# Kernel tuning notes

Hardware: AMD Instinct MI355X
Metric: run time of the kernel (lower is better)

The kernel has to match this reference:

```python
import jax, jax.numpy as jnp
import numpy as np

N_NODES = 50000
N_EDGES = 600000
IC, H, OC = 64, 128, 32
EPS = 1e-5


def setup_inputs() -> dict:
    key = jax.random.key(0)
    ks = jax.random.split(key, 8)
    x = jax.random.normal(ks[0], (N_NODES, IC), dtype=jnp.float32)
    ei = jax.random.randint(ks[1], (2, N_EDGES), 0, N_NODES, dtype=jnp.int64)
    proj_w = jax.random.normal(ks[2], (IC, H), dtype=jnp.float32) * 0.05
    proj_b = jnp.zeros((H,), dtype=jnp.float32)
    # conv_w[layer, lin, :, :] with lin order: key, query, value, skip
    conv_w = jax.random.normal(ks[3], (3, 4, H, H), dtype=jnp.float32) * 0.05
    conv_b = jnp.zeros((3, 4, H), dtype=jnp.float32)
    bn_gamma = jnp.ones((3, H), dtype=jnp.float32)
    bn_beta = jnp.zeros((3, H), dtype=jnp.float32)
    head_w = jax.random.normal(ks[4], (H, OC), dtype=jnp.float32) * 0.05
    head_b = jnp.zeros((OC,), dtype=jnp.float32)
    return {"x": x, "ei": ei, "proj_w": proj_w, "proj_b": proj_b,
            "conv_w": conv_w, "conv_b": conv_b, "bn_gamma": bn_gamma,
            "bn_beta": bn_beta, "head_w": head_w, "head_b": head_b}


def _res_gated_conv(x, src, dst, w, b):
    # PyG ResGatedGraphConv: out_i = skip(x_i) + sum_j sigmoid(key(x_i)+query(x_j)) * value(x_j)
    k = x @ w[0] + b[0]      # key   (applied to target/dst)
    q = x @ w[1] + b[1]      # query (applied to source/src)
    v = x @ w[2] + b[2]      # value (applied to source/src)
    msg = jax.nn.sigmoid(k[dst] + q[src]) * v[src]          # [E, H]
    agg = jax.ops.segment_sum(msg, dst, num_segments=x.shape[0])  # [N, H]
    return x @ w[3] + b[3] + agg


def _batchnorm(x, gamma, beta):
    # training-mode BatchNorm1d: batch statistics over the node dimension
    mean = jnp.mean(x, axis=0)
    var = jnp.var(x, axis=0)
    return gamma * (x - mean) * jax.lax.rsqrt(var + EPS) + beta


def reference(x, ei, proj_w, proj_b, conv_w, conv_b, bn_gamma, bn_beta, head_w, head_b):
    src, dst = ei[0], ei[1]
    h = jax.nn.relu(x @ proj_w + proj_b)
    for layer in range(3):
        h = _res_gated_conv(h, src, dst, conv_w[layer], conv_b[layer])
        h = jax.nn.relu(_batchnorm(h, bn_gamma[layer], bn_beta[layer]))
        # dropout(p=0.2) is identity in eval mode
    return h @ head_w + head_b
```

## Files before the change

kernel.cpp:

```cpp
#include <hip/hip_runtime.h>
#include <hip/hip_bf16.h>
#include <math.h>

#define HDIM 128
#define ICDIM 64
#define OCDIM 32
#define BN_EPS 1e-5f
#define NCH 64
#define NCHG 128

typedef __attribute__((ext_vector_type(8))) short bv8;
typedef __attribute__((ext_vector_type(4))) float fv4;

static __device__ __forceinline__ unsigned short f2bf(float v) {
    __hip_bfloat16 t = __float2bfloat16(v);
    return *(unsigned short*)&t;
}
static __device__ __forceinline__ float bflo(unsigned int u) {
    union { unsigned int i; float f; } c; c.i = u << 16; return c.f;
}
static __device__ __forceinline__ float bfhi(unsigned int u) {
    union { unsigned int i; float f; } c; c.i = u & 0xffff0000u; return c.f;
}
static __device__ __forceinline__ unsigned int pack2bf(float a, float b) {
    return (unsigned int)f2bf(a) | ((unsigned int)f2bf(b) << 16);
}

__global__ void wprep_kernel(const float* __restrict__ conv_w,
                             const float* __restrict__ proj_w,
                             __hip_bfloat16* __restrict__ Wt,
                             __hip_bfloat16* __restrict__ Wp) {
    int mat = blockIdx.x;
    if (mat < 12) {
        const float* s = conv_w + (size_t)mat * HDIM * HDIM;
        __hip_bfloat16* d = Wt + (size_t)mat * HDIM * HDIM;
        for (int idx = threadIdx.x; idx < HDIM * HDIM; idx += 256) {
            int i = idx >> 7, o = idx & 127;
            d[(size_t)o * HDIM + i] = __float2bfloat16(s[idx]);
        }
    } else {
        for (int idx = threadIdx.x; idx < ICDIM * HDIM; idx += 256) {
            int i = idx >> 7, o = idx & 127;
            Wp[(size_t)o * ICDIM + i] = __float2bfloat16(proj_w[idx]);
        }
    }
}

__global__ __launch_bounds__(256)
void proj_mfma_kernel(const float* __restrict__ x,
                      const __hip_bfloat16* __restrict__ wp,
                      const float* __restrict__ b,
                      __hip_bfloat16* __restrict__ h, int n) {
    __shared__ unsigned int xs[NCH * ICDIM / 2];
    int tid = threadIdx.x;
    int m0 = blockIdx.x * NCH;

    const float2* xsrc = (const float2*)(x + (size_t)m0 * ICDIM);
    for (int i = tid; i < NCH * ICDIM / 2; i += 256) {
        int node = m0 + (i >> 5);
        float2 v = (node < n) ? xsrc[i] : (float2){0.f, 0.f};
        xs[i ^ (((i >> 5) & 7) << 2)] = pack2bf(v.x, v.y);
    }

    int wv = tid >> 6;
    int lane = tid & 63;
    int j = lane & 15;
    int kg = lane >> 4;
    int sw = (j & 7) << 4;

    bv8 af[2][2];
#pragma unroll
    for (int gs = 0; gs < 2; ++gs)
#pragma unroll
        for (int ks = 0; ks < 2; ++ks)
            af[gs][ks] = *(const bv8*)((const unsigned short*)wp +
                (size_t)(wv * 32 + gs * 16 + j) * ICDIM + ks * 32 + kg * 8);

    float4 bias0 = *(const float4*)(b + wv * 32 + kg * 4);
    float4 bias1 = *(const float4*)(b + wv * 32 + 16 + kg * 4);

    __syncthreads();

#pragma unroll
    for (int t4 = 0; t4 < NCH / 16; ++t4) {
        const char* rowbase = (const char*)xs + (t4 * 16 + j) * (ICDIM * 2);
        fv4 acc0 = (fv4){0.f, 0.f, 0.f, 0.f};
        fv4 acc1 = (fv4){0.f, 0.f, 0.f, 0.f};
#pragma unroll
        for (int ks = 0; ks < 2; ++ks) {
            bv8 bf = *(const bv8*)(rowbase + ((kg * 16 + ks * 64) ^ sw));
            acc0 = __builtin_amdgcn_mfma_f32_16x16x32_bf16(af[0][ks], bf, acc0, 0, 0, 0);
            acc1 = __builtin_amdgcn_mfma_f32_16x16x32_bf16(af[1][ks], bf, acc1, 0, 0, 0);
        }
        int node = m0 + t4 * 16 + j;
        if (node < n) {
            unsigned short* o =
                (unsigned short*)h + (size_t)node * HDIM + wv * 32 + kg * 4;
            ushort4 r0, r1;
            r0.x = f2bf(fmaxf(acc0.x + bias0.x, 0.f));
            r0.y = f2bf(fmaxf(acc0.y + bias0.y, 0.f));
            r0.z = f2bf(fmaxf(acc0.z + bias0.z, 0.f));
            r0.w = f2bf(fmaxf(acc0.w + bias0.w, 0.f));
            r1.x = f2bf(fmaxf(acc1.x + bias1.x, 0.f));
            r1.y = f2bf(fmaxf(acc1.y + bias1.y, 0.f));
            r1.z = f2bf(fmaxf(acc1.z + bias1.z, 0.f));
            r1.w = f2bf(fmaxf(acc1.w + bias1.w, 0.f));
            *(ushort4*)o = r0;
            *(ushort4*)(o + 16) = r1;
        }
    }
}

__global__ __launch_bounds__(1024)
void gemm4_fused_kernel(const __hip_bfloat16* __restrict__ hB,
                        const float* __restrict__ Ssrc,
                        const float* __restrict__ stp,
                        const float* __restrict__ gma,
                        const float* __restrict__ bta,
                        const __hip_bfloat16* __restrict__ wt4,
                        const float* __restrict__ b4,
                        __hip_bfloat16* __restrict__ K,
                        unsigned int* __restrict__ QV,
                        float* __restrict__ S, int n) {
    __shared__ unsigned short hs[NCHG * HDIM];
    int tid = threadIdx.x;
    int m0 = blockIdx.x * NCHG;

    if (Ssrc) {
        const float4* src = (const float4*)(Ssrc + (size_t)m0 * HDIM);
        float invn = 1.f / (float)n;
#pragma unroll
        for (int it = 0; it < 2; ++it) {
            int idx = it * 1024 + tid;
            float4 v0 = src[idx * 2];
            float4 v1 = src[idx * 2 + 1];
            int c0 = (idx * 8) & 127;
            float vv[8] = {v0.x, v0.y, v0.z, v0.w, v1.x, v1.y, v1.z, v1.w};
            int wsw = ((idx >> 4) & 7) << 4;
            unsigned int* dst = (unsigned int*)((char*)hs + ((idx * 16) ^ wsw));
#pragma unroll
            for (int p = 0; p < 8; p += 2) {
                int c = c0 + p;
                float mA = stp[c] * invn, mB = stp[c + 1] * invn;
                float scA = gma[c] * rsqrtf(stp[128 + c] * invn - mA * mA + BN_EPS);
                float scB = gma[c + 1] * rsqrtf(stp[129 + c] * invn - mB * mB + BN_EPS);
                float shA = bta[c] - mA * scA, shB = bta[c + 1] - mB * scB;
                float rA = fmaxf(fmaf(vv[p], scA, shA), 0.f);
                float rB = fmaxf(fmaf(vv[p + 1], scB, shB), 0.f);
                dst[p >> 1] = pack2bf(rA, rB);
            }
        }
    } else {
        const uint4* src = (const uint4*)((const unsigned short*)hB + (size_t)m0 * HDIM);
#pragma unroll
        for (int it = 0; it < 2; ++it) {
            int idx = it * 1024 + tid;
            int wsw = ((idx >> 4) & 7) << 4;
            *(uint4*)((char*)hs + ((idx * 16) ^ wsw)) = src[idx];
        }
    }

    int wv = tid >> 6;
    int lane = tid & 63;
    int lin = wv >> 2;
    int g2 = wv & 3;
    int j = lane & 15;
    int kg = lane >> 4;
    int sw = (j & 7) << 4;

    const unsigned short* wbase =
        (const unsigned short*)(wt4 + (size_t)lin * HDIM * HDIM);
    bv8 af[2][4];
#pragma unroll
    for (int gs = 0; gs < 2; ++gs)
#pragma unroll
        for (int ks = 0; ks < 4; ++ks)
            af[gs][ks] = *(const bv8*)(wbase +
                (size_t)(g2 * 32 + gs * 16 + j) * HDIM + ks * 32 + kg * 8);

    const float* bl = b4 + lin * HDIM;
    float4 bias0 = *(const float4*)(bl + g2 * 32 + kg * 4);
    float4 bias1 = *(const float4*)(bl + g2 * 32 + 16 + kg * 4);

    __syncthreads();

#pragma unroll
    for (int t4 = 0; t4 < NCHG / 16; ++t4) {
        const char* rowbase = (const char*)hs + (t4 * 16 + j) * (HDIM * 2);
        fv4 acc0 = (fv4){0.f, 0.f, 0.f, 0.f};
        fv4 acc1 = (fv4){0.f, 0.f, 0.f, 0.f};
#pragma unroll
        for (int ks = 0; ks < 4; ++ks) {
            bv8 bf = *(const bv8*)(rowbase + ((kg * 16 + ks * 64) ^ sw));
            acc0 = __builtin_amdgcn_mfma_f32_16x16x32_bf16(af[0][ks], bf, acc0, 0, 0, 0);
            acc1 = __builtin_amdgcn_mfma_f32_16x16x32_bf16(af[1][ks], bf, acc1, 0, 0, 0);
        }
        int node = m0 + t4 * 16 + j;
        if (node >= n) continue;
        int c0 = g2 * 32 + kg * 4;
        float f0 = acc0.x + bias0.x, f1 = acc0.y + bias0.y;
        float f2 = acc0.z + bias0.z, f3 = acc0.w + bias0.w;
        float f4 = acc1.x + bias1.x, f5 = acc1.y + bias1.y;
        float f6 = acc1.z + bias1.z, f7 = acc1.w + bias1.w;
        if (lin == 3) {
            float* o = S + (size_t)node * HDIM + c0;
            *(float4*)o = (float4){f0, f1, f2, f3};
            *(float4*)(o + 16) = (float4){f4, f5, f6, f7};
        } else if (lin == 0) {
            unsigned short* o = (unsigned short*)K + (size_t)node * HDIM + c0;
            *(ushort4*)o = (ushort4){f2bf(f0), f2bf(f1), f2bf(f2), f2bf(f3)};
            *(ushort4*)(o + 16) = (ushort4){f2bf(f4), f2bf(f5), f2bf(f6), f2bf(f7)};
        } else {
            unsigned short* o = (unsigned short*)QV + (size_t)node * 256 + 2 * c0
                              + ((lin == 2) ? 4 : 0);
            *(ushort4*)o = (ushort4){f2bf(f0), f2bf(f1), f2bf(f2), f2bf(f3)};
            *(ushort4*)(o + 32) = (ushort4){f2bf(f4), f2bf(f5), f2bf(f6), f2bf(f7)};
        }
    }
}

__global__ void hist_kernel(const int* __restrict__ ei, int* __restrict__ deg, int e) {
    int i = blockIdx.x * 256 + threadIdx.x;
    if (i < e) atomicAdd(&deg[ei[(size_t)e + i]], 1);
}

__global__ void scan1_kernel(const int* __restrict__ deg, int* __restrict__ incl,
                             int* __restrict__ bsum, int n) {
    __shared__ int tmp[256];
    int i = blockIdx.x * 256 + threadIdx.x;
    int v = (i < n) ? deg[i] : 0;
    tmp[threadIdx.x] = v;
    __syncthreads();
    for (int ofs = 1; ofs < 256; ofs <<= 1) {
        int t = (threadIdx.x >= ofs) ? tmp[threadIdx.x - ofs] : 0;
        __syncthreads();
        tmp[threadIdx.x] += t;
        __syncthreads();
    }
    if (i < n) incl[i] = tmp[threadIdx.x];
    if (threadIdx.x == 255) bsum[blockIdx.x] = tmp[255];
}

__global__ void scan23_kernel(const int* __restrict__ deg, const int* __restrict__ incl,
                              const int* __restrict__ bsum, int* __restrict__ off,
                              int* __restrict__ cursor, int n, int e, int nb) {
    __shared__ int tmp[256];
    int t = threadIdx.x;
    tmp[t] = (t < nb) ? bsum[t] : 0;
    __syncthreads();
    for (int ofs = 1; ofs < 256; ofs <<= 1) {
        int a = (t >= ofs) ? tmp[t - ofs] : 0;
        __syncthreads();
        tmp[t] += a;
        __syncthreads();
    }
    int pre = (blockIdx.x == 0) ? 0 : tmp[blockIdx.x - 1];
    int i = blockIdx.x * 256 + t;
    if (i < n) {
        int ex = incl[i] - deg[i] + pre;
        off[i] = ex;
        cursor[i] = ex;
        if (i == n - 1) off[n] = e;
    }
}

__global__ void scatter_kernel(const int* __restrict__ ei, int* __restrict__ cursor,
                               int* __restrict__ esrc, int e) {
    int i = blockIdx.x * 256 + threadIdx.x;
    if (i < e) {
        int dst = ei[(size_t)e + i];
        int pos = atomicAdd(&cursor[dst], 1);
        esrc[pos] = ei[i];
    }
}

__global__ void agg_kernel(const int* __restrict__ off, const int* __restrict__ esrc,
                           const __hip_bfloat16* __restrict__ kb,
                           const unsigned int* __restrict__ QV,
                           float* __restrict__ S, int n) {
    int d = blockIdx.x * 4 + (threadIdx.x >> 6);
    if (d >= n) return;
    int lane = threadIdx.x & 63;
    int half = lane >> 5;
    int cl = lane & 31;
    const char* qvb = (const char*)QV;

    uint2 ku = *(const uint2*)((const unsigned short*)kb + (size_t)d * HDIM + 4 * cl);
    float k0 = bflo(ku.x), k1 = bfhi(ku.x), k2 = bflo(ku.y), k3 = bfhi(ku.y);
    float a0 = 0.f, a1 = 0.f, a2 = 0.f, a3 = 0.f;

#define EDGE4(u)                                                     \
    {                                                                \
        float g0 = k0 + bflo(u.x), g1 = k1 + bfhi(u.x);              \
        float g2 = k2 + bflo(u.y), g3 = k3 + bfhi(u.y);              \
        a0 += __fdividef(bflo(u.z), 1.f + __expf(-g0));              \
        a1 += __fdividef(bfhi(u.z), 1.f + __expf(-g1));              \
        a2 += __fdividef(bflo(u.w), 1.f + __expf(-g2));              \
        a3 += __fdividef(bfhi(u.w), 1.f + __expf(-g3));              \
    }

    int j = off[d] + half, s1 = off[d + 1];
    for (; j + 2 < s1; j += 4) {
        int sA = esrc[j], sB = esrc[j + 2];
        uint4 uA = *(const uint4*)(qvb + (size_t)sA * 512 + cl * 16);
        uint4 uB = *(const uint4*)(qvb + (size_t)sB * 512 + cl * 16);
        EDGE4(uA);
        EDGE4(uB);
    }
    if (j < s1) {
        int sA = esrc[j];
        uint4 uA = *(const uint4*)(qvb + (size_t)sA * 512 + cl * 16);
        EDGE4(uA);
    }
#undef EDGE4

    a0 += __shfl_xor(a0, 32);
    a1 += __shfl_xor(a1, 32);
    a2 += __shfl_xor(a2, 32);
    a3 += __shfl_xor(a3, 32);
    if (half == 0) {
        float4* sp = (float4*)(S + (size_t)d * HDIM) + cl;
        float4 o = *sp;
        o.x += a0; o.y += a1; o.z += a2; o.w += a3;
        *sp = o;
    }
}

__global__ void stats_kernel(const float* __restrict__ s,
                             float* __restrict__ stats, int n) {
    int c = threadIdx.x & 127, rh = threadIdx.x >> 7;
    int r0 = blockIdx.x * 128;
    int r1 = min(r0 + 128, n);
    float sum = 0.f, sq = 0.f;
    for (int r = r0 + rh; r < r1; r += 2) {
        float v = s[(size_t)r * HDIM + c];
        sum += v;
        sq = fmaf(v, v, sq);
    }
    __shared__ float ls[2][HDIM], lq[2][HDIM];
    ls[rh][c] = sum;
    lq[rh][c] = sq;
    __syncthreads();
    if (rh == 0) {
        atomicAdd(&stats[c], ls[0][c] + ls[1][c]);
        atomicAdd(&stats[HDIM + c], lq[0][c] + lq[1][c]);
    }
}

__global__ void head_bn_kernel(const float* __restrict__ S,
                               const float* __restrict__ stats,
                               const float* __restrict__ gamma,
                               const float* __restrict__ beta,
                               const float* __restrict__ w,
                               const float* __restrict__ b,
                               float* __restrict__ out, int n) {
    __shared__ float hsm[8][HDIM];
    float invn = 1.f / (float)n;
    for (int i = threadIdx.x; i < 8 * HDIM; i += 256) {
        int r = i >> 7, c = i & 127;
        int node = blockIdx.x * 8 + r;
        float v = 0.f;
        if (node < n) {
            float mean = stats[c] * invn;
            float var = stats[128 + c] * invn - mean * mean;
            float sc = gamma[c] * rsqrtf(var + BN_EPS);
            float sh = beta[c] - mean * sc;
            v = fmaxf(fmaf(S[(size_t)node * HDIM + c], sc, sh), 0.f);
        }
        hsm[r][c] = v;
    }
    __syncthreads();
    int c = threadIdx.x & 31;
    int ng = threadIdx.x >> 5;
    int node = blockIdx.x * 8 + ng;
    if (node >= n) return;
    float acc = b[c];
#pragma unroll
    for (int k = 0; k < HDIM; ++k)
        acc = fmaf(hsm[ng][k], w[k * OCDIM + c], acc);
    out[(size_t)node * OCDIM + c] = acc;
}

extern "C" void kernel_launch(void* const* d_in, const int* in_sizes, int n_in,
                              void* d_out, int out_size, void* d_ws, size_t ws_size,
                              hipStream_t stream) {
    const float* x      = (const float*)d_in[0];
    const int*   ei     = (const int*)  d_in[1];
    const float* proj_w = (const float*)d_in[2];
    const float* proj_b = (const float*)d_in[3];
    const float* conv_w = (const float*)d_in[4];
    const float* conv_b = (const float*)d_in[5];
    const float* bn_g   = (const float*)d_in[6];
    const float* bn_b   = (const float*)d_in[7];
    const float* head_w = (const float*)d_in[8];
    const float* head_b = (const float*)d_in[9];
    float* out = (float*)d_out;

    int n = in_sizes[0] / ICDIM;
    int e = in_sizes[1] / 2;

    size_t nh = (size_t)n * HDIM;
    size_t need = nh * 4 + 768 * 4 + nh * 2 + nh * 2 + nh * 4
                + (size_t)12 * HDIM * HDIM * 2 + (size_t)HDIM * ICDIM * 2
                + ((size_t)3 * n + (n + 1) + 256 + e) * 4;
    if (ws_size < need) return;

    float* S  = (float*)d_ws;
    float* st = S + nh;
    __hip_bfloat16* h = (__hip_bfloat16*)(st + 768);
    __hip_bfloat16* K = h + nh;
    unsigned int* QV = (unsigned int*)(K + nh);
    __hip_bfloat16* Wt = (__hip_bfloat16*)(QV + nh);
    __hip_bfloat16* Wp = Wt + (size_t)12 * HDIM * HDIM;

    int* deg    = (int*)(Wp + (size_t)HDIM * ICDIM);
    int* incl   = deg + n;
    int* off    = incl + n;
    int* cursor = off + n + 1;
    int* bsum   = cursor + n;
    int* esrc   = bsum + 256;

    hipMemsetAsync(st, 0, 768 * sizeof(float), stream);
    hipMemsetAsync(deg, 0, (size_t)n * sizeof(int), stream);

    int gb_e = (e + 255) / 256;
    int gb_n = (n + 255) / 256;

    wprep_kernel<<<13, 256, 0, stream>>>(conv_w, proj_w, Wt, Wp);
    proj_mfma_kernel<<<(n + NCH - 1) / NCH, 256, 0, stream>>>(x, Wp, proj_b, h, n);

    hist_kernel<<<gb_e, 256, 0, stream>>>(ei, deg, e);
    scan1_kernel<<<gb_n, 256, 0, stream>>>(deg, incl, bsum, n);
    scan23_kernel<<<gb_n, 256, 0, stream>>>(deg, incl, bsum, off, cursor, n, e, gb_n);
    scatter_kernel<<<gb_e, 256, 0, stream>>>(ei, cursor, esrc, e);

    int gm = (n + NCHG - 1) / NCHG;
    for (int l = 0; l < 3; ++l) {
        const float* Ssrc = (l == 0) ? nullptr : S;
        const float* stp  = (l == 0) ? st : st + (size_t)(l - 1) * 256;
        const float* gma  = (l == 0) ? bn_g : bn_g + (size_t)(l - 1) * HDIM;
        const float* bta  = (l == 0) ? bn_b : bn_b + (size_t)(l - 1) * HDIM;
        gemm4_fused_kernel<<<gm, 1024, 0, stream>>>(
            h, Ssrc, stp, gma, bta,
            Wt + (size_t)l * 4 * HDIM * HDIM, conv_b + (size_t)l * 4 * HDIM,
            K, QV, S, n);
        agg_kernel<<<(n + 3) / 4, 256, 0, stream>>>(off, esrc, K, QV, S, n);
        stats_kernel<<<(n + 127) / 128, 256, 0, stream>>>(S, st + l * 256, n);
    }

    head_bn_kernel<<<(n + 7) / 8, 256, 0, stream>>>(
        S, st + 2 * 256, bn_g + 2 * HDIM, bn_b + 2 * HDIM, head_w, head_b, out, n);
}
```

Baseline: 465.9 us.

## Store pre-BatchNorm activations S in bf16 instead of fp32

The skip/aggregate buffer S changes from fp32 to bf16 throughout: the gemm writes it as bf16, the aggregation does a bf16 read-modify-write, and the stats, next-layer gemm and head kernels read bf16. This halves the memory traffic on the largest intermediate across several kernels per layer. The cost is extra rounding: the skip output is rounded before the aggregate is added, and the result is rounded again, which may reduce accuracy in the BatchNorm statistics.

```diff
diff --git a/kernel.cpp b/kernel.cpp
--- a/kernel.cpp
+++ b/kernel.cpp
@@ -113,7 +113,7 @@
 
 __global__ __launch_bounds__(1024)
 void gemm4_fused_kernel(const __hip_bfloat16* __restrict__ hB,
-                        const float* __restrict__ Ssrc,
+                        const __hip_bfloat16* __restrict__ Ssrc,
                         const float* __restrict__ stp,
                         const float* __restrict__ gma,
                         const float* __restrict__ bta,
@@ -121,21 +121,21 @@
                         const float* __restrict__ b4,
                         __hip_bfloat16* __restrict__ K,
                         unsigned int* __restrict__ QV,
-                        float* __restrict__ S, int n) {
+                        __hip_bfloat16* __restrict__ S, int n) {
     __shared__ unsigned short hs[NCHG * HDIM];
     int tid = threadIdx.x;
     int m0 = blockIdx.x * NCHG;
 
     if (Ssrc) {
-        const float4* src = (const float4*)(Ssrc + (size_t)m0 * HDIM);
+        const uint4* src = (const uint4*)Ssrc;
         float invn = 1.f / (float)n;
 #pragma unroll
         for (int it = 0; it < 2; ++it) {
             int idx = it * 1024 + tid;
-            float4 v0 = src[idx * 2];
-            float4 v1 = src[idx * 2 + 1];
+            uint4 u = src[(size_t)blockIdx.x * 2048 + idx];
             int c0 = (idx * 8) & 127;
-            float vv[8] = {v0.x, v0.y, v0.z, v0.w, v1.x, v1.y, v1.z, v1.w};
+            float vv[8] = {bflo(u.x), bfhi(u.x), bflo(u.y), bfhi(u.y),
+                           bflo(u.z), bfhi(u.z), bflo(u.w), bfhi(u.w)};
             int wsw = ((idx >> 4) & 7) << 4;
             unsigned int* dst = (unsigned int*)((char*)hs + ((idx * 16) ^ wsw));
 #pragma unroll
@@ -203,9 +203,9 @@
         float f4 = acc1.x + bias1.x, f5 = acc1.y + bias1.y;
         float f6 = acc1.z + bias1.z, f7 = acc1.w + bias1.w;
         if (lin == 3) {
-            float* o = S + (size_t)node * HDIM + c0;
-            *(float4*)o = (float4){f0, f1, f2, f3};
-            *(float4*)(o + 16) = (float4){f4, f5, f6, f7};
+            unsigned short* o = (unsigned short*)S + (size_t)node * HDIM + c0;
+            *(ushort4*)o = (ushort4){f2bf(f0), f2bf(f1), f2bf(f2), f2bf(f3)};
+            *(ushort4*)(o + 16) = (ushort4){f2bf(f4), f2bf(f5), f2bf(f6), f2bf(f7)};
         } else if (lin == 0) {
             unsigned short* o = (unsigned short*)K + (size_t)node * HDIM + c0;
             *(ushort4*)o = (ushort4){f2bf(f0), f2bf(f1), f2bf(f2), f2bf(f3)};
@@ -277,7 +277,7 @@
 __global__ void agg_kernel(const int* __restrict__ off, const int* __restrict__ esrc,
                            const __hip_bfloat16* __restrict__ kb,
                            const unsigned int* __restrict__ QV,
-                           float* __restrict__ S, int n) {
+                           __hip_bfloat16* __restrict__ S, int n) {
     int d = blockIdx.x * 4 + (threadIdx.x >> 6);
     if (d >= n) return;
     int lane = threadIdx.x & 63;
@@ -319,35 +319,45 @@
     a2 += __shfl_xor(a2, 32);
     a3 += __shfl_xor(a3, 32);
     if (half == 0) {
-        float4* sp = (float4*)(S + (size_t)d * HDIM) + cl;
-        float4 o = *sp;
-        o.x += a0; o.y += a1; o.z += a2; o.w += a3;
-        *sp = o;
-    }
-}
-
-__global__ void stats_kernel(const float* __restrict__ s,
+        unsigned int* sp = (unsigned int*)S + (size_t)d * 64 + 2 * cl;
+        uint2 o = *(uint2*)sp;
+        float b0 = bflo(o.x) + a0, b1 = bfhi(o.x) + a1;
+        float b2 = bflo(o.y) + a2, b3 = bfhi(o.y) + a3;
+        uint2 w2;
+        w2.x = pack2bf(b0, b1);
+        w2.y = pack2bf(b2, b3);
+        *(uint2*)sp = w2;
+    }
+}
+
+__global__ void stats_kernel(const __hip_bfloat16* __restrict__ s,
                              float* __restrict__ stats, int n) {
-    int c = threadIdx.x & 127, rh = threadIdx.x >> 7;
+    int c2 = threadIdx.x & 63;
+    int rh = threadIdx.x >> 6;
     int r0 = blockIdx.x * 128;
     int r1 = min(r0 + 128, n);
-    float sum = 0.f, sq = 0.f;
-    for (int r = r0 + rh; r < r1; r += 2) {
-        float v = s[(size_t)r * HDIM + c];
-        sum += v;
-        sq = fmaf(v, v, sq);
-    }
-    __shared__ float ls[2][HDIM], lq[2][HDIM];
-    ls[rh][c] = sum;
-    lq[rh][c] = sq;
-    __syncthreads();
-    if (rh == 0) {
-        atomicAdd(&stats[c], ls[0][c] + ls[1][c]);
-        atomicAdd(&stats[HDIM + c], lq[0][c] + lq[1][c]);
-    }
-}
-
-__global__ void head_bn_kernel(const float* __restrict__ S,
+    const unsigned int* sw = (const unsigned int*)s;
+    float s0 = 0.f, s1 = 0.f, q0 = 0.f, q1 = 0.f;
+    for (int r = r0 + rh; r < r1; r += 4) {
+        unsigned int u = sw[(size_t)r * 64 + c2];
+        float a = bflo(u), b = bfhi(u);
+        s0 += a; q0 = fmaf(a, a, q0);
+        s1 += b; q1 = fmaf(b, b, q1);
+    }
+    __shared__ float ls[4][128], lq[4][128];
+    ls[rh][2 * c2] = s0; ls[rh][2 * c2 + 1] = s1;
+    lq[rh][2 * c2] = q0; lq[rh][2 * c2 + 1] = q1;
+    __syncthreads();
+    int t = threadIdx.x;
+    if (t < 128) {
+        atomicAdd(&stats[t], ls[0][t] + ls[1][t] + ls[2][t] + ls[3][t]);
+    } else {
+        int c = t - 128;
+        atomicAdd(&stats[128 + c], lq[0][c] + lq[1][c] + lq[2][c] + lq[3][c]);
+    }
+}
+
+__global__ void head_bn_kernel(const __hip_bfloat16* __restrict__ S,
                                const float* __restrict__ stats,
                                const float* __restrict__ gamma,
                                const float* __restrict__ beta,
@@ -356,18 +366,27 @@
                                float* __restrict__ out, int n) {
     __shared__ float hsm[8][HDIM];
     float invn = 1.f / (float)n;
-    for (int i = threadIdx.x; i < 8 * HDIM; i += 256) {
-        int r = i >> 7, c = i & 127;
+    const unsigned int* sw = (const unsigned int*)S;
+    for (int wd = threadIdx.x; wd < 8 * 64; wd += 256) {
+        int r = wd >> 6, c2 = wd & 63;
         int node = blockIdx.x * 8 + r;
-        float v = 0.f;
+        float v0 = 0.f, v1 = 0.f;
         if (node < n) {
-            float mean = stats[c] * invn;
-            float var = stats[128 + c] * invn - mean * mean;
-            float sc = gamma[c] * rsqrtf(var + BN_EPS);
-            float sh = beta[c] - mean * sc;
-            v = fmaxf(fmaf(S[(size_t)node * HDIM + c], sc, sh), 0.f);
-        }
-        hsm[r][c] = v;
+            unsigned int u = sw[(size_t)node * 64 + c2];
+            int c = 2 * c2;
+            float m0 = stats[c] * invn;
+            float var0 = stats[128 + c] * invn - m0 * m0;
+            float sc0 = gamma[c] * rsqrtf(var0 + BN_EPS);
+            float sh0 = beta[c] - m0 * sc0;
+            v0 = fmaxf(fmaf(bflo(u), sc0, sh0), 0.f);
+            float m1 = stats[c + 1] * invn;
+            float var1 = stats[129 + c] * invn - m1 * m1;
+            float sc1 = gamma[c + 1] * rsqrtf(var1 + BN_EPS);
+            float sh1 = beta[c + 1] - m1 * sc1;
+            v1 = fmaxf(fmaf(bfhi(u), sc1, sh1), 0.f);
+        }
+        hsm[r][2 * c2] = v0;
+        hsm[r][2 * c2 + 1] = v1;
     }
     __syncthreads();
     int c = threadIdx.x & 31;
@@ -400,13 +419,13 @@
     int e = in_sizes[1] / 2;
 
     size_t nh = (size_t)n * HDIM;
-    size_t need = nh * 4 + 768 * 4 + nh * 2 + nh * 2 + nh * 4
+    size_t need = nh * 2 + 768 * 4 + nh * 2 + nh * 2 + nh * 4
                 + (size_t)12 * HDIM * HDIM * 2 + (size_t)HDIM * ICDIM * 2
                 + ((size_t)3 * n + (n + 1) + 256 + e) * 4;
     if (ws_size < need) return;
 
-    float* S  = (float*)d_ws;
-    float* st = S + nh;
+    __hip_bfloat16* S = (__hip_bfloat16*)d_ws;
+    float* st = (float*)(S + nh);
     __hip_bfloat16* h = (__hip_bfloat16*)(st + 768);
     __hip_bfloat16* K = h + nh;
     unsigned int* QV = (unsigned int*)(K + nh);
@@ -436,7 +455,7 @@
 
     int gm = (n + NCHG - 1) / NCHG;
     for (int l = 0; l < 3; ++l) {
-        const float* Ssrc = (l == 0) ? nullptr : S;
+        const __hip_bfloat16* Ssrc = (l == 0) ? nullptr : S;
         const float* stp  = (l == 0) ? st : st + (size_t)(l - 1) * 256;
         const float* gma  = (l == 0) ? bn_g : bn_g + (size_t)(l - 1) * HDIM;
         const float* bta  = (l == 0) ? bn_b : bn_b + (size_t)(l - 1) * HDIM;
```

New measurement: 445.7 us. 1.05x faster.
